# Kernel optimization log

Measured on AMD Instinct MI355X. Metric: run time of the kernel, lower is better.

Reference implementation:

```python
import jax, jax.numpy as jnp
import numpy as np

N = 40000
E = 640000
F_IN = 128
HID = 64
HEADS = 4
NUM_CLASSES = 40
NEG_SLOPE = 0.2  # GATConv default leaky_relu slope


def setup_inputs() -> dict:
    key = jax.random.key(0)
    ks = jax.random.split(key, 10)
    glorot = lambda k, shape: (jax.random.uniform(k, shape, jnp.float32) * 2.0 - 1.0) * jnp.sqrt(6.0 / (shape[0] + shape[-1]))
    x = jax.random.normal(ks[0], (N, F_IN), jnp.float32)
    edge_index = jax.random.randint(ks[1], (2, E), 0, N, jnp.int64)
    # layer 1: in=128 -> heads=4, out=64, concat
    W1 = glorot(ks[2], (F_IN, HEADS * HID))
    att_src1 = glorot(ks[3], (HEADS, HID))
    att_dst1 = glorot(ks[4], (HEADS, HID))
    b1 = jnp.zeros((HEADS * HID,), jnp.float32)
    # layer 2: in=256 -> heads=1, out=num_classes
    W2 = glorot(ks[5], (HEADS * HID, 1 * NUM_CLASSES))
    att_src2 = glorot(ks[6], (1, NUM_CLASSES))
    att_dst2 = glorot(ks[7], (1, NUM_CLASSES))
    b2 = jnp.zeros((NUM_CLASSES,), jnp.float32)
    return {"x": x, "edge_index": edge_index, "W1": W1, "att_src1": att_src1,
            "att_dst1": att_dst1, "b1": b1, "W2": W2, "att_src2": att_src2,
            "att_dst2": att_dst2, "b2": b2}


def gat_conv(x, src, dst, W, att_src, att_dst, bias, heads, out_ch, n_nodes):
    """PyG GATConv (add_self_loops applied by caller, dropout=eval/no-op)."""
    h = (x @ W).reshape(n_nodes, heads, out_ch)            # [N, H, C]
    a_src = jnp.einsum('nhc,hc->nh', h, att_src)            # [N, H]
    a_dst = jnp.einsum('nhc,hc->nh', h, att_dst)            # [N, H]
    e = jax.nn.leaky_relu(a_src[src] + a_dst[dst], NEG_SLOPE)  # [E', H]
    # segment softmax over incoming edges of each destination node
    m = jax.ops.segment_max(e, dst, num_segments=n_nodes)   # [N, H]
    p = jnp.exp(e - m[dst])
    z = jax.ops.segment_sum(p, dst, num_segments=n_nodes)   # [N, H]
    alpha = p / z[dst]                                      # [E', H]
    msg = h[src] * alpha[:, :, None]                        # [E', H, C]
    out = jax.ops.segment_sum(msg, dst, num_segments=n_nodes)  # [N, H, C]
    return out.reshape(n_nodes, heads * out_ch) + bias


def reference(x, edge_index, W1, att_src1, att_dst1, b1, W2, att_src2, att_dst2, b2):
    loop = jnp.arange(N, dtype=edge_index.dtype)
    src = jnp.concatenate([edge_index[0], loop])
    dst = jnp.concatenate([edge_index[1], loop])
    h = gat_conv(x, src, dst, W1, att_src1, att_dst1, b1, HEADS, HID, N)
    h = jax.nn.relu(h)  # dropout is identity in eval mode
    h = gat_conv(h, src, dst, W2, att_src2, att_dst2, b2, 1, NUM_CLASSES, N)
    return jax.nn.log_softmax(h, axis=1)
```

## Files before the change

kernel.cpp:

```cpp
#include <hip/hip_runtime.h>
#include <math.h>

#define NEG_SLOPE 0.2f

typedef unsigned short ushort_t;
typedef __attribute__((ext_vector_type(8))) short short8v;
typedef __attribute__((ext_vector_type(4))) float f32x4;

__device__ inline ushort_t f2bf(float f) {
    unsigned b = __float_as_uint(f);
    unsigned r = (b + 0x7fffu + ((b >> 16) & 1u)) >> 16;
    return (ushort_t)r;
}
__device__ inline float bf2f(ushort_t u) { return __uint_as_float(((unsigned)u) << 16); }
__device__ inline float bflo(unsigned w) { return __uint_as_float(w << 16); }
__device__ inline float bfhi(unsigned w) { return __uint_as_float(w & 0xffff0000u); }

__global__ void hist_prepack_kernel(const int* __restrict__ ei, int E, int EP,
                                    int* __restrict__ deg,
                                    const float* __restrict__ W1, const float* __restrict__ W2,
                                    ushort_t* __restrict__ w1p, ushort_t* __restrict__ w2p)
{
    int e = blockIdx.x * 256 + threadIdx.x;
    if (e < EP) {
        int d = (e < E) ? ei[E + e] : (e - E);
        atomicAdd(&deg[d], 1);
    }
    if (e < 32768) {
        int j = e & 7, lane = (e >> 3) & 63, t = e >> 9;
        int kt = t >> 4, nt = t & 15;
        int k = kt * 32 + (lane >> 4) * 8 + j;
        int n = nt * 16 + (lane & 15);
        w1p[e] = f2bf(W1[k * 256 + n]);
    } else if (e < 32768 + 12288) {
        int ii = e - 32768;
        int j = ii & 7, lane = (ii >> 3) & 63, t = ii >> 9;
        int kt = t / 3, nt = t - kt * 3;
        int k = kt * 32 + (lane >> 4) * 8 + j;
        int n = nt * 16 + (lane & 15);
        w2p[ii] = (n < 40) ? f2bf(W2[k * 40 + n]) : (ushort_t)0;
    }
}

__global__ void block_sum_kernel(const int* __restrict__ deg, int* __restrict__ bsum, int N)
{
    int i = blockIdx.x * 256 + threadIdx.x;
    int v = (i < N) ? deg[i] : 0;
#pragma unroll
    for (int off = 32; off > 0; off >>= 1) v += __shfl_xor(v, off, 64);
    __shared__ int wsum[4];
    if ((threadIdx.x & 63) == 0) wsum[threadIdx.x >> 6] = v;
    __syncthreads();
    if (threadIdx.x == 0) bsum[blockIdx.x] = wsum[0] + wsum[1] + wsum[2] + wsum[3];
}

__global__ void block_scan_kernel(const int* __restrict__ deg, const int* __restrict__ bsum,
                                  int* __restrict__ rowptr, int N, int nb)
{
    __shared__ int sb[256];
    __shared__ int sh[256];
    const int tid = threadIdx.x;
    int bv = (tid < nb) ? bsum[tid] : 0;
    sb[tid] = bv;
    int i = blockIdx.x * 256 + tid;
    int v = (i < N) ? deg[i] : 0;
    sh[tid] = v;
    __syncthreads();
    for (int off = 1; off < 256; off <<= 1) {
        int tb = (tid >= off) ? sb[tid - off] : 0;
        int tv = (tid >= off) ? sh[tid - off] : 0;
        __syncthreads();
        sb[tid] += tb;
        sh[tid] += tv;
        __syncthreads();
    }
    int blkoff = (blockIdx.x == 0) ? 0 : sb[blockIdx.x - 1];
    if (i < N) rowptr[i] = blkoff + sh[tid] - v;
    if (blockIdx.x == 0 && tid == 0) rowptr[N] = sb[nb - 1];
}

__global__ void scatter_kernel(const int* __restrict__ ei, int E, int EP,
                               const int* __restrict__ rowptr, int* __restrict__ deg,
                               int* __restrict__ colsrc)
{
    int e = blockIdx.x * 256 + threadIdx.x;
    if (e >= EP) return;
    int s, d;
    if (e < E) { s = ei[e]; d = ei[E + e]; } else { s = e - E; d = e - E; }
    int old = atomicSub(&deg[d], 1);
    colsrc[rowptr[d] + old - 1] = s;
}

__global__ __launch_bounds__(256) void gemm1_mfma(
    const float* __restrict__ x, const ushort_t* __restrict__ w1p,
    const float* __restrict__ att_src, const float* __restrict__ att_dst,
    ushort_t* __restrict__ h1b, float* __restrict__ asrc, float* __restrict__ adst, int N)
{
    __shared__ ushort_t xs[64][136];
    const int n0 = blockIdx.x * 64;
    const int tid = threadIdx.x;
    const int lane = tid & 63;
    const int w = tid >> 6;
    const int l16 = lane & 15;
    const int g = lane >> 4;

#pragma unroll
    for (int it = 0; it < 8; it++) {
        int idx = tid + it * 256;
        int row = idx >> 5, c4 = (idx & 31) * 4;
        float4 v = *(const float4*)(x + (size_t)(n0 + row) * 128 + c4);
        ushort4 u = {f2bf(v.x), f2bf(v.y), f2bf(v.z), f2bf(v.w)};
        *(ushort4*)&xs[row][c4] = u;
    }
    __syncthreads();

    short8v afr[4];
#pragma unroll
    for (int kt = 0; kt < 4; kt++)
        afr[kt] = *(const short8v*)&xs[w * 16 + l16][kt * 32 + g * 8];

    f32x4 acc[16];
#pragma unroll
    for (int nt = 0; nt < 16; nt++) acc[nt] = (f32x4){0.f, 0.f, 0.f, 0.f};

    const short8v* wp = (const short8v*)w1p;
#pragma unroll
    for (int nt = 0; nt < 16; nt++) {
        short8v b0 = wp[(0 * 16 + nt) * 64 + lane];
        short8v b1 = wp[(1 * 16 + nt) * 64 + lane];
        short8v b2 = wp[(2 * 16 + nt) * 64 + lane];
        short8v b3 = wp[(3 * 16 + nt) * 64 + lane];
        acc[nt] = __builtin_amdgcn_mfma_f32_16x16x32_bf16(afr[0], b0, acc[nt], 0, 0, 0);
        acc[nt] = __builtin_amdgcn_mfma_f32_16x16x32_bf16(afr[1], b1, acc[nt], 0, 0, 0);
        acc[nt] = __builtin_amdgcn_mfma_f32_16x16x32_bf16(afr[2], b2, acc[nt], 0, 0, 0);
        acc[nt] = __builtin_amdgcn_mfma_f32_16x16x32_bf16(afr[3], b3, acc[nt], 0, 0, 0);
    }

    float ps[4][4], pd[4][4];
#pragma unroll
    for (int r = 0; r < 4; r++)
#pragma unroll
        for (int h = 0; h < 4; h++) { ps[r][h] = 0.f; pd[r][h] = 0.f; }

#pragma unroll
    for (int nt = 0; nt < 16; nt++) {
        const int col = nt * 16 + l16;
        const float as_c = att_src[col];
        const float ad_c = att_dst[col];
        const int h = nt >> 2;
#pragma unroll
        for (int r = 0; r < 4; r++) {
            float v = acc[nt][r];
            h1b[(size_t)(n0 + w * 16 + g * 4 + r) * 256 + col] = f2bf(v);
            ps[r][h] += v * as_c;
            pd[r][h] += v * ad_c;
        }
    }
#pragma unroll
    for (int r = 0; r < 4; r++)
#pragma unroll
        for (int h = 0; h < 4; h++)
#pragma unroll
            for (int off = 8; off > 0; off >>= 1) {
                ps[r][h] += __shfl_xor(ps[r][h], off, 64);
                pd[r][h] += __shfl_xor(pd[r][h], off, 64);
            }

    const int sel = l16 >> 2;
#pragma unroll
    for (int hh = 0; hh < 4; hh++) {
        if (hh == (l16 & 3)) {
            if (sel == 0) {
#pragma unroll
                for (int r = 0; r < 4; r++)
                    asrc[(size_t)(n0 + w * 16 + g * 4 + r) * 4 + hh] = ps[r][hh];
            } else if (sel == 1) {
#pragma unroll
                for (int r = 0; r < 4; r++)
                    adst[(size_t)(n0 + w * 16 + g * 4 + r) * 4 + hh] = pd[r][hh];
            }
        }
    }
}

__global__ __launch_bounds__(256) void node_agg1(
    const int* __restrict__ rowptr, const int* __restrict__ colsrc,
    const float* __restrict__ asrc, const float* __restrict__ adst,
    const ushort_t* __restrict__ h1b, const float* __restrict__ b1,
    ushort_t* __restrict__ a1b, int N)
{
    int n = (blockIdx.x * 256 + threadIdx.x) >> 6;
    int lane = threadIdx.x & 63;
    if (n >= N) return;
    const int r0 = rowptr[n], r1 = rowptr[n + 1];
    const int half = lane >> 5;
    const int l5 = lane & 31;
    const int head = l5 >> 3;
    const int coff = head * 64 + (l5 & 7) * 8;
    const float adhh = adst[(size_t)n * 4 + head];

    float acc[8] = {0.f, 0.f, 0.f, 0.f, 0.f, 0.f, 0.f, 0.f};
    float ssum = 0.f;
    int j = r0;
    for (; j + 8 <= r1; j += 8) {
        int jA = j + half, jB = j + 2 + half, jC = j + 4 + half, jD = j + 6 + half;
        int sA = colsrc[jA], sB = colsrc[jB], sC = colsrc[jC], sD = colsrc[jD];
        float aA = asrc[(size_t)sA * 4 + head];
        float aB = asrc[(size_t)sB * 4 + head];
        float aC = asrc[(size_t)sC * 4 + head];
        float aD = asrc[(size_t)sD * 4 + head];
        uint4 qA = *(const uint4*)&h1b[(size_t)sA * 256 + coff];
        uint4 qB = *(const uint4*)&h1b[(size_t)sB * 256 + coff];
        uint4 qC = *(const uint4*)&h1b[(size_t)sC * 256 + coff];
        uint4 qD = *(const uint4*)&h1b[(size_t)sD * 256 + coff];
        float vA = aA + adhh; vA = vA > 0.f ? vA : NEG_SLOPE * vA;
        float vB = aB + adhh; vB = vB > 0.f ? vB : NEG_SLOPE * vB;
        float vC = aC + adhh; vC = vC > 0.f ? vC : NEG_SLOPE * vC;
        float vD = aD + adhh; vD = vD > 0.f ? vD : NEG_SLOPE * vD;
        float pA = __expf(vA), pB = __expf(vB), pC = __expf(vC), pD = __expf(vD);
        ssum += (pA + pB) + (pC + pD);
        acc[0] += pA * bflo(qA.x) + pB * bflo(qB.x) + pC * bflo(qC.x) + pD * bflo(qD.x);
        acc[1] += pA * bfhi(qA.x) + pB * bfhi(qB.x) + pC * bfhi(qC.x) + pD * bfhi(qD.x);
        acc[2] += pA * bflo(qA.y) + pB * bflo(qB.y) + pC * bflo(qC.y) + pD * bflo(qD.y);
        acc[3] += pA * bfhi(qA.y) + pB * bfhi(qB.y) + pC * bfhi(qC.y) + pD * bfhi(qD.y);
        acc[4] += pA * bflo(qA.z) + pB * bflo(qB.z) + pC * bflo(qC.z) + pD * bflo(qD.z);
        acc[5] += pA * bfhi(qA.z) + pB * bfhi(qB.z) + pC * bfhi(qC.z) + pD * bfhi(qD.z);
        acc[6] += pA * bflo(qA.w) + pB * bflo(qB.w) + pC * bflo(qC.w) + pD * bflo(qD.w);
        acc[7] += pA * bfhi(qA.w) + pB * bfhi(qB.w) + pC * bfhi(qC.w) + pD * bfhi(qD.w);
    }
    for (; j < r1; j += 2) {
        int jj = j + half;
        bool valid = jj < r1;
        int s = colsrc[valid ? jj : r0];
        float a = asrc[(size_t)s * 4 + head];
        uint4 q = *(const uint4*)&h1b[(size_t)s * 256 + coff];
        float v = a + adhh; v = v > 0.f ? v : NEG_SLOPE * v;
        float p = valid ? __expf(v) : 0.f;
        ssum += p;
        acc[0] += p * bflo(q.x);
        acc[1] += p * bfhi(q.x);
        acc[2] += p * bflo(q.y);
        acc[3] += p * bfhi(q.y);
        acc[4] += p * bflo(q.z);
        acc[5] += p * bfhi(q.z);
        acc[6] += p * bflo(q.w);
        acc[7] += p * bfhi(q.w);
    }

#pragma unroll
    for (int k = 0; k < 8; k++) acc[k] += __shfl_xor(acc[k], 32, 64);
    ssum += __shfl_xor(ssum, 32, 64);
    const float rz = 1.f / ssum;

    float s0 = half ? acc[4] : acc[0];
    float s1 = half ? acc[5] : acc[1];
    float s2 = half ? acc[6] : acc[2];
    float s3 = half ? acc[7] : acc[3];
    const int wc = coff + half * 4;
    const float4 bv = *(const float4*)&b1[wc];
    float o0 = s0 * rz + bv.x;
    float o1 = s1 * rz + bv.y;
    float o2 = s2 * rz + bv.z;
    float o3 = s3 * rz + bv.w;
    ushort4 outv = {f2bf(o0 > 0.f ? o0 : 0.f), f2bf(o1 > 0.f ? o1 : 0.f),
                    f2bf(o2 > 0.f ? o2 : 0.f), f2bf(o3 > 0.f ? o3 : 0.f)};
    *(ushort4*)&a1b[(size_t)n * 256 + wc] = outv;
}

__global__ __launch_bounds__(256) void gemm2_mfma(
    const ushort_t* __restrict__ A, const ushort_t* __restrict__ w2p,
    const float* __restrict__ as2, const float* __restrict__ ad2,
    ushort_t* __restrict__ h2b, float* __restrict__ asrc, float* __restrict__ adst, int N)
{
    __shared__ ushort_t xs[64][264];
    const int n0 = blockIdx.x * 64;
    const int tid = threadIdx.x;
    const int lane = tid & 63;
    const int w = tid >> 6;
    const int l16 = lane & 15;
    const int g = lane >> 4;

#pragma unroll
    for (int it = 0; it < 8; it++) {
        int idx = tid + it * 256;
        int row = idx >> 5, c8 = (idx & 31) * 8;
        uint4 v = *(const uint4*)(A + (size_t)(n0 + row) * 256 + c8);
        *(uint4*)&xs[row][c8] = v;
    }
    __syncthreads();

    short8v afr[8];
#pragma unroll
    for (int kt = 0; kt < 8; kt++)
        afr[kt] = *(const short8v*)&xs[w * 16 + l16][kt * 32 + g * 8];

    f32x4 acc[3];
#pragma unroll
    for (int nt = 0; nt < 3; nt++) acc[nt] = (f32x4){0.f, 0.f, 0.f, 0.f};

    const short8v* wp = (const short8v*)w2p;
#pragma unroll
    for (int nt = 0; nt < 3; nt++) {
#pragma unroll
        for (int kt = 0; kt < 8; kt++) {
            short8v b = wp[(kt * 3 + nt) * 64 + lane];
            acc[nt] = __builtin_amdgcn_mfma_f32_16x16x32_bf16(afr[kt], b, acc[nt], 0, 0, 0);
        }
    }

    float ps[4] = {0.f, 0.f, 0.f, 0.f}, pd[4] = {0.f, 0.f, 0.f, 0.f};
#pragma unroll
    for (int nt = 0; nt < 3; nt++) {
        const int col = nt * 16 + l16;
        const bool ok = col < 40;
        const float as_c = ok ? as2[col] : 0.f;
        const float ad_c = ok ? ad2[col] : 0.f;
#pragma unroll
        for (int r = 0; r < 4; r++) {
            float v = acc[nt][r];
            if (ok) h2b[(size_t)(n0 + w * 16 + g * 4 + r) * 40 + col] = f2bf(v);
            ps[r] += v * as_c;
            pd[r] += v * ad_c;
        }
    }
#pragma unroll
    for (int r = 0; r < 4; r++)
#pragma unroll
        for (int off = 8; off > 0; off >>= 1) {
            ps[r] += __shfl_xor(ps[r], off, 64);
            pd[r] += __shfl_xor(pd[r], off, 64);
        }
    if (l16 == 0) {
#pragma unroll
        for (int r = 0; r < 4; r++) asrc[n0 + w * 16 + g * 4 + r] = ps[r];
    } else if (l16 == 1) {
#pragma unroll
        for (int r = 0; r < 4; r++) adst[n0 + w * 16 + g * 4 + r] = pd[r];
    }
}

__global__ __launch_bounds__(256) void node_agg2(
    const int* __restrict__ rowptr, const int* __restrict__ colsrc,
    const float* __restrict__ asrc, const float* __restrict__ adst,
    const ushort_t* __restrict__ h2b, const float* __restrict__ b2,
    float* __restrict__ out, int N)
{
    int n = (blockIdx.x * 256 + threadIdx.x) >> 6;
    int lane = threadIdx.x & 63;
    if (n >= N) return;
    const int r0 = rowptr[n], r1 = rowptr[n + 1];
    const int half = lane >> 5;
    const int l5 = lane & 31;
    const bool act = l5 < 20;
    const int cc = act ? 2 * l5 : 0;
    const float ad = adst[n];

    float acc0 = 0.f, acc1 = 0.f, ssum = 0.f;
    int j = r0;
    for (; j + 8 <= r1; j += 8) {
        int jA = j + half, jB = j + 2 + half, jC = j + 4 + half, jD = j + 6 + half;
        int sA = colsrc[jA], sB = colsrc[jB], sC = colsrc[jC], sD = colsrc[jD];
        float eA = asrc[sA] + ad, eB = asrc[sB] + ad, eC = asrc[sC] + ad, eD = asrc[sD] + ad;
        unsigned qA = *(const unsigned*)&h2b[(size_t)sA * 40 + cc];
        unsigned qB = *(const unsigned*)&h2b[(size_t)sB * 40 + cc];
        unsigned qC = *(const unsigned*)&h2b[(size_t)sC * 40 + cc];
        unsigned qD = *(const unsigned*)&h2b[(size_t)sD * 40 + cc];
        eA = eA > 0.f ? eA : NEG_SLOPE * eA;
        eB = eB > 0.f ? eB : NEG_SLOPE * eB;
        eC = eC > 0.f ? eC : NEG_SLOPE * eC;
        eD = eD > 0.f ? eD : NEG_SLOPE * eD;
        float pA = __expf(eA), pB = __expf(eB), pC = __expf(eC), pD = __expf(eD);
        ssum += (pA + pB) + (pC + pD);
        acc0 += pA * bflo(qA) + pB * bflo(qB) + pC * bflo(qC) + pD * bflo(qD);
        acc1 += pA * bfhi(qA) + pB * bfhi(qB) + pC * bfhi(qC) + pD * bfhi(qD);
    }
    for (; j < r1; j += 2) {
        int jj = j + half;
        bool valid = jj < r1;
        int s = colsrc[valid ? jj : r0];
        float e = asrc[s] + ad;
        unsigned q = *(const unsigned*)&h2b[(size_t)s * 40 + cc];
        e = e > 0.f ? e : NEG_SLOPE * e;
        float p = valid ? __expf(e) : 0.f;
        ssum += p;
        acc0 += p * bflo(q);
        acc1 += p * bfhi(q);
    }

    acc0 += __shfl_xor(acc0, 32, 64);
    acc1 += __shfl_xor(acc1, 32, 64);
    ssum += __shfl_xor(ssum, 32, 64);
    const float rz = 1.f / ssum;

    float v0 = act ? acc0 * rz + b2[cc]     : -1.0e30f;
    float v1 = act ? acc1 * rz + b2[cc + 1] : -1.0e30f;
    float mx = fmaxf(v0, v1);
#pragma unroll
    for (int off = 16; off > 0; off >>= 1) mx = fmaxf(mx, __shfl_xor(mx, off, 64));
    float pe = act ? __expf(v0 - mx) + __expf(v1 - mx) : 0.f;
#pragma unroll
    for (int off = 16; off > 0; off >>= 1) pe += __shfl_xor(pe, off, 64);
    float lse = mx + logf(pe);
    if (act && half == 0) {
        float2 o = make_float2(v0 - lse, v1 - lse);
        *(float2*)&out[(size_t)n * 40 + cc] = o;
    }
}

extern "C" void kernel_launch(void* const* d_in, const int* in_sizes, int n_in,
                              void* d_out, int out_size, void* d_ws, size_t ws_size,
                              hipStream_t stream)
{
    const float* x   = (const float*)d_in[0];
    const int*   ei  = (const int*)d_in[1];
    const float* W1  = (const float*)d_in[2];
    const float* as1 = (const float*)d_in[3];
    const float* ad1 = (const float*)d_in[4];
    const float* b1  = (const float*)d_in[5];
    const float* W2  = (const float*)d_in[6];
    const float* as2 = (const float*)d_in[7];
    const float* ad2 = (const float*)d_in[8];
    const float* b2  = (const float*)d_in[9];
    float* out = (float*)d_out;

    const int N  = in_sizes[0] / 128;
    const int E  = in_sizes[1] / 2;
    const int EP = E + N;
    const int NB = (N + 255) / 256;

    char* ws = (char*)d_ws;
    ushort_t* h1b  = (ushort_t*)ws;
    ushort_t* a1b  = h1b + (size_t)N * 256;
    float* asrc    = (float*)(a1b + (size_t)N * 256);
    float* adst    = asrc + (size_t)N * 4;
    int*   rowptr  = (int*)(adst + (size_t)N * 4);
    int*   colsrc  = rowptr + (N + 1);
    int*   deg     = colsrc + EP;
    ushort_t* h2b  = (ushort_t*)(deg + N);
    int*   bsum    = (int*)(h2b + (size_t)N * 40 + 16);
    ushort_t* w1p  = (ushort_t*)(bsum + NB);
    ushort_t* w2p  = w1p + 32768;

    hipMemsetAsync(deg, 0, (size_t)N * sizeof(int), stream);
    int egrid = (EP + 255) / 256;
    hist_prepack_kernel<<<egrid, 256, 0, stream>>>(ei, E, EP, deg, W1, W2, w1p, w2p);
    block_sum_kernel<<<NB, 256, 0, stream>>>(deg, bsum, N);
    block_scan_kernel<<<NB, 256, 0, stream>>>(deg, bsum, rowptr, N, NB);
    scatter_kernel<<<egrid, 256, 0, stream>>>(ei, E, EP, rowptr, deg, colsrc);

    gemm1_mfma<<<N / 64, 256, 0, stream>>>(x, w1p, as1, ad1, h1b, asrc, adst, N);
    node_agg1<<<(N * 64 + 255) / 256, 256, 0, stream>>>(rowptr, colsrc, asrc, adst, h1b, b1, a1b, N);

    gemm2_mfma<<<N / 64, 256, 0, stream>>>(a1b, w2p, as2, ad2, h2b, asrc, adst, N);
    node_agg2<<<(N * 64 + 255) / 256, 256, 0, stream>>>(rowptr, colsrc, asrc, adst, h2b, b2, out, N);
}
```

Before: 182.3 us.

## Fuse CSR build stages into one cooperative kernel with grid syncs

Replaces the memset, histogram/prepack, block-sum, block-scan and scatter launches with a single cooperative kernel of 1024 blocks that uses grid-wide syncs between phases. The goal is to remove per-launch overhead and inter-kernel gaps in the CSR construction. In exchange it adds five grid barriers, grid-stride loops, and a single-block scan of the block sums, and it depends on all 1024 blocks being co-resident for the cooperative launch.

Result: slower. 653.0 us (+258.3%).

```diff
diff --git a/kernel.cpp b/kernel.cpp
--- a/kernel.cpp
+++ b/kernel.cpp
@@ -1,5 +1,8 @@
 #include <hip/hip_runtime.h>
+#include <hip/hip_cooperative_groups.h>
 #include <math.h>
+
+namespace cg = cooperative_groups;
 
 #define NEG_SLOPE 0.2f
 
@@ -16,79 +19,94 @@
 __device__ inline float bflo(unsigned w) { return __uint_as_float(w << 16); }
 __device__ inline float bfhi(unsigned w) { return __uint_as_float(w & 0xffff0000u); }
 
-__global__ void hist_prepack_kernel(const int* __restrict__ ei, int E, int EP,
-                                    int* __restrict__ deg,
-                                    const float* __restrict__ W1, const float* __restrict__ W2,
-                                    ushort_t* __restrict__ w1p, ushort_t* __restrict__ w2p)
-{
-    int e = blockIdx.x * 256 + threadIdx.x;
-    if (e < EP) {
+__global__ __launch_bounds__(256) void csr_coop_kernel(
+    const int* __restrict__ ei, int E, int EP, int N, int NB,
+    const float* __restrict__ W1, const float* __restrict__ W2,
+    ushort_t* __restrict__ w1p, ushort_t* __restrict__ w2p,
+    int* __restrict__ deg, int* __restrict__ bsum,
+    int* __restrict__ rowptr, int* __restrict__ colsrc)
+{
+    cg::grid_group grid = cg::this_grid();
+    __shared__ int wsum[4];
+    __shared__ int sh[256];
+    const int tid = threadIdx.x;
+    const int gsz = gridDim.x * 256;
+    const int gidx = blockIdx.x * 256 + tid;
+
+    for (int i = gidx; i < N; i += gsz) deg[i] = 0;
+    grid.sync();
+
+    for (int e = gidx; e < EP; e += gsz) {
         int d = (e < E) ? ei[E + e] : (e - E);
         atomicAdd(&deg[d], 1);
     }
-    if (e < 32768) {
-        int j = e & 7, lane = (e >> 3) & 63, t = e >> 9;
-        int kt = t >> 4, nt = t & 15;
-        int k = kt * 32 + (lane >> 4) * 8 + j;
-        int n = nt * 16 + (lane & 15);
-        w1p[e] = f2bf(W1[k * 256 + n]);
-    } else if (e < 32768 + 12288) {
-        int ii = e - 32768;
-        int j = ii & 7, lane = (ii >> 3) & 63, t = ii >> 9;
-        int kt = t / 3, nt = t - kt * 3;
-        int k = kt * 32 + (lane >> 4) * 8 + j;
-        int n = nt * 16 + (lane & 15);
-        w2p[ii] = (n < 40) ? f2bf(W2[k * 40 + n]) : (ushort_t)0;
-    }
-}
-
-__global__ void block_sum_kernel(const int* __restrict__ deg, int* __restrict__ bsum, int N)
-{
-    int i = blockIdx.x * 256 + threadIdx.x;
-    int v = (i < N) ? deg[i] : 0;
-#pragma unroll
-    for (int off = 32; off > 0; off >>= 1) v += __shfl_xor(v, off, 64);
-    __shared__ int wsum[4];
-    if ((threadIdx.x & 63) == 0) wsum[threadIdx.x >> 6] = v;
-    __syncthreads();
-    if (threadIdx.x == 0) bsum[blockIdx.x] = wsum[0] + wsum[1] + wsum[2] + wsum[3];
-}
-
-__global__ void block_scan_kernel(const int* __restrict__ deg, const int* __restrict__ bsum,
-                                  int* __restrict__ rowptr, int N, int nb)
-{
-    __shared__ int sb[256];
-    __shared__ int sh[256];
-    const int tid = threadIdx.x;
-    int bv = (tid < nb) ? bsum[tid] : 0;
-    sb[tid] = bv;
-    int i = blockIdx.x * 256 + tid;
-    int v = (i < N) ? deg[i] : 0;
-    sh[tid] = v;
-    __syncthreads();
-    for (int off = 1; off < 256; off <<= 1) {
-        int tb = (tid >= off) ? sb[tid - off] : 0;
-        int tv = (tid >= off) ? sh[tid - off] : 0;
+    for (int i = gidx; i < 32768 + 12288; i += gsz) {
+        if (i < 32768) {
+            int j = i & 7, lane = (i >> 3) & 63, t = i >> 9;
+            int kt = t >> 4, nt = t & 15;
+            int k = kt * 32 + (lane >> 4) * 8 + j;
+            int n = nt * 16 + (lane & 15);
+            w1p[i] = f2bf(W1[k * 256 + n]);
+        } else {
+            int ii = i - 32768;
+            int j = ii & 7, lane = (ii >> 3) & 63, t = ii >> 9;
+            int kt = t / 3, nt = t - kt * 3;
+            int k = kt * 32 + (lane >> 4) * 8 + j;
+            int n = nt * 16 + (lane & 15);
+            w2p[ii] = (n < 40) ? f2bf(W2[k * 40 + n]) : (ushort_t)0;
+        }
+    }
+    grid.sync();
+
+    for (int b = blockIdx.x; b < NB; b += gridDim.x) {
+        int i = b * 256 + tid;
+        int v = (i < N) ? deg[i] : 0;
+#pragma unroll
+        for (int off = 32; off > 0; off >>= 1) v += __shfl_xor(v, off, 64);
+        if ((tid & 63) == 0) wsum[tid >> 6] = v;
         __syncthreads();
-        sb[tid] += tb;
-        sh[tid] += tv;
+        if (tid == 0) bsum[b] = wsum[0] + wsum[1] + wsum[2] + wsum[3];
         __syncthreads();
     }
-    int blkoff = (blockIdx.x == 0) ? 0 : sb[blockIdx.x - 1];
-    if (i < N) rowptr[i] = blkoff + sh[tid] - v;
-    if (blockIdx.x == 0 && tid == 0) rowptr[N] = sb[nb - 1];
-}
-
-__global__ void scatter_kernel(const int* __restrict__ ei, int E, int EP,
-                               const int* __restrict__ rowptr, int* __restrict__ deg,
-                               int* __restrict__ colsrc)
-{
-    int e = blockIdx.x * 256 + threadIdx.x;
-    if (e >= EP) return;
-    int s, d;
-    if (e < E) { s = ei[e]; d = ei[E + e]; } else { s = e - E; d = e - E; }
-    int old = atomicSub(&deg[d], 1);
-    colsrc[rowptr[d] + old - 1] = s;
+    grid.sync();
+
+    if (blockIdx.x == 0) {
+        int v = (tid < NB) ? bsum[tid] : 0;
+        sh[tid] = v;
+        __syncthreads();
+        for (int off = 1; off < 256; off <<= 1) {
+            int t = (tid >= off) ? sh[tid - off] : 0;
+            __syncthreads();
+            sh[tid] += t;
+            __syncthreads();
+        }
+        if (tid < NB) bsum[tid] = sh[tid] - v;
+        if (tid == 0) rowptr[N] = sh[255];
+    }
+    grid.sync();
+
+    for (int b = blockIdx.x; b < NB; b += gridDim.x) {
+        int i = b * 256 + tid;
+        int v = (i < N) ? deg[i] : 0;
+        sh[tid] = v;
+        __syncthreads();
+        for (int off = 1; off < 256; off <<= 1) {
+            int t = (tid >= off) ? sh[tid - off] : 0;
+            __syncthreads();
+            sh[tid] += t;
+            __syncthreads();
+        }
+        if (i < N) rowptr[i] = bsum[b] + sh[tid] - v;
+        __syncthreads();
+    }
+    grid.sync();
+
+    for (int e = gidx; e < EP; e += gsz) {
+        int s, d;
+        if (e < E) { s = ei[e]; d = ei[E + e]; } else { s = e - E; d = e - E; }
+        int old = atomicSub(&deg[d], 1);
+        colsrc[rowptr[d] + old - 1] = s;
+    }
 }
 
 __global__ __launch_bounds__(256) void gemm1_mfma(
@@ -441,12 +459,22 @@
     ushort_t* w1p  = (ushort_t*)(bsum + NB);
     ushort_t* w2p  = w1p + 32768;
 
-    hipMemsetAsync(deg, 0, (size_t)N * sizeof(int), stream);
-    int egrid = (EP + 255) / 256;
-    hist_prepack_kernel<<<egrid, 256, 0, stream>>>(ei, E, EP, deg, W1, W2, w1p, w2p);
-    block_sum_kernel<<<NB, 256, 0, stream>>>(deg, bsum, N);
-    block_scan_kernel<<<NB, 256, 0, stream>>>(deg, bsum, rowptr, N, NB);
-    scatter_kernel<<<egrid, 256, 0, stream>>>(ei, E, EP, rowptr, deg, colsrc);
+    {
+        int E_ = E, EP_ = EP, N_ = N, NB_ = NB;
+        const int* ei_ = ei;
+        const float* W1_ = W1;
+        const float* W2_ = W2;
+        ushort_t* w1p_ = w1p;
+        ushort_t* w2p_ = w2p;
+        int* deg_ = deg;
+        int* bsum_ = bsum;
+        int* rowptr_ = rowptr;
+        int* colsrc_ = colsrc;
+        void* args[] = {&ei_, &E_, &EP_, &N_, &NB_, &W1_, &W2_,
+                        &w1p_, &w2p_, &deg_, &bsum_, &rowptr_, &colsrc_};
+        hipLaunchCooperativeKernel((const void*)csr_coop_kernel,
+                                   dim3(1024), dim3(256), args, 0, stream);
+    }
 
     gemm1_mfma<<<N / 64, 256, 0, stream>>>(x, w1p, as1, ad1, h1b, asrc, adst, N);
     node_agg1<<<(N * 64 + 255) / 256, 256, 0, stream>>>(rowptr, colsrc, asrc, adst, h1b, b1, a1b, N);
```
